# Performance work log

Measured on AMD Instinct MI355X. Metric: run time of the kernel, lower is better.

## Reference

```python
import jax, jax.numpy as jnp
import numpy as np

N, K, M = 1024, 256, 1024
INIT_SCALE = 0.1


def setup_inputs() -> dict:
    key = jax.random.key(0)
    kx, kw = jax.random.split(key)
    x = jax.random.normal(kx, (N, K), dtype=jnp.float32)
    weight = jax.random.normal(kw, (M, K), dtype=jnp.float32) * INIT_SCALE
    return {"x": x, "weight": weight}


def reference(x, weight):
    # Tropical (max-plus) matmul: out[n, m] = max_k(|x[n, k]| + |w[m, k]|)
    ax = jnp.abs(x)        # [N, K]
    aw = jnp.abs(weight)   # [M, K]
    # broadcast to [N, M, K] then reduce over K (mirrors the original expand+add+max)
    return jnp.max(ax[:, None, :] + aw[None, :, :], axis=2)  # [N, M]
```

## Files before the change

### kernel.cpp

```cpp
#include <hip/hip_runtime.h>


typedef float v2f __attribute__((ext_vector_type(2)));
typedef float v4f __attribute__((ext_vector_type(4)));

constexpr int TILE  = 32;
constexpr int KB    = 64;
constexpr int KKP   = KB / 2;
constexpr int PITCH = TILE + 2;

__global__ void __launch_bounds__(256)
tropical_kernel(const float* __restrict__ xg, const float* __restrict__ wg,
                float* __restrict__ outg)
{
    constexpr int K = 256;
    constexpr int M = 1024;

    __shared__ __align__(16) v2f xs[KKP * PITCH];
    __shared__ __align__(16) v2f ws[KKP * PITCH];

    const int tid = threadIdx.x;
    const int tx = tid & 15;
    const int ty = tid >> 4;
    const int bn = (int)(blockIdx.x >> 5) * TILE;
    const int bm = (int)(blockIdx.x & 31) * TILE;

    const int r = tid >> 3;
    const int c = (tid & 7) * 8;
    const float* xbase = xg + (bn + r) * K + c;
    const float* wbase = wg + (bm + r) * K + c;

    v4f xr0 = *(const v4f*)(xbase);
    v4f xr1 = *(const v4f*)(xbase + 4);
    v4f wr0 = *(const v4f*)(wbase);
    v4f wr1 = *(const v4f*)(wbase + 4);

    float a00 = 0.f, a01 = 0.f, a10 = 0.f, a11 = 0.f;

    const int kp = c >> 1;

    for (int chunk = 0; chunk < K / KB; ++chunk) {
        __syncthreads();
        xs[(kp + 0) * PITCH + r] = (v2f){fabsf(xr0.x), fabsf(xr0.y)};
        xs[(kp + 1) * PITCH + r] = (v2f){fabsf(xr0.z), fabsf(xr0.w)};
        xs[(kp + 2) * PITCH + r] = (v2f){fabsf(xr1.x), fabsf(xr1.y)};
        xs[(kp + 3) * PITCH + r] = (v2f){fabsf(xr1.z), fabsf(xr1.w)};
        ws[(kp + 0) * PITCH + r] = (v2f){fabsf(wr0.x), fabsf(wr0.y)};
        ws[(kp + 1) * PITCH + r] = (v2f){fabsf(wr0.z), fabsf(wr0.w)};
        ws[(kp + 2) * PITCH + r] = (v2f){fabsf(wr1.x), fabsf(wr1.y)};
        ws[(kp + 3) * PITCH + r] = (v2f){fabsf(wr1.z), fabsf(wr1.w)};
        __syncthreads();

        if (chunk + 1 < K / KB) {
            const float* xn = xbase + (chunk + 1) * KB;
            const float* wn = wbase + (chunk + 1) * KB;
            xr0 = *(const v4f*)(xn);
            xr1 = *(const v4f*)(xn + 4);
            wr0 = *(const v4f*)(wn);
            wr1 = *(const v4f*)(wn + 4);
        }

#pragma unroll
        for (int kk = 0; kk < KKP; ++kk) {
            v4f xv = *(const v4f*)&xs[kk * PITCH + 2 * ty];
            v4f wv = *(const v4f*)&ws[kk * PITCH + 2 * tx];
            v2f x0 = {xv.x, xv.y}, x1 = {xv.z, xv.w};
            v2f w0 = {wv.x, wv.y}, w1 = {wv.z, wv.w};
            v2f s;
            s = x0 + w0; a00 = fmaxf(a00, fmaxf(s.x, s.y));
            s = x0 + w1; a01 = fmaxf(a01, fmaxf(s.x, s.y));
            s = x1 + w0; a10 = fmaxf(a10, fmaxf(s.x, s.y));
            s = x1 + w1; a11 = fmaxf(a11, fmaxf(s.x, s.y));
        }
    }

    const int n0 = bn + 2 * ty;
    const int m0 = bm + 2 * tx;
    *(v2f*)(outg + n0 * M + m0)       = (v2f){a00, a01};
    *(v2f*)(outg + (n0 + 1) * M + m0) = (v2f){a10, a11};
}

extern "C" void kernel_launch(void* const* d_in, const int* in_sizes, int n_in,
                              void* d_out, int out_size, void* d_ws, size_t ws_size,
                              hipStream_t stream)
{
    const float* x = (const float*)d_in[0];
    const float* w = (const float*)d_in[1];
    float* out = (float*)d_out;

    dim3 grid(1024);
    dim3 block(256);
    tropical_kernel<<<grid, block, 0, stream>>>(x, w, out);
}
```

Baseline: 71.13 us.

## Use 64x64 tiles with 4x4 per-thread outputs and full-K XOR-swizzled LDS

Block tile grows from 32x32 to 64x64, and each thread now computes a 4x4 output micro-tile instead of 2x2. The whole K=256 slice of x and w is staged into LDS once, with an XOR swizzle in place of padding, so the chunked K loop and its repeated barriers go away. This raises arithmetic intensity per LDS read and cuts synchronization. In exchange, LDS per block reaches 128KB, the grid drops to 256 blocks, and occupancy is limited to one block per CU.

Result: slower. 72.57 us (+2.0%).

```diff
diff --git a/kernel.cpp b/kernel.cpp
--- a/kernel.cpp
+++ b/kernel.cpp
@@ -4,80 +4,100 @@
 typedef float v2f __attribute__((ext_vector_type(2)));
 typedef float v4f __attribute__((ext_vector_type(4)));
 
-constexpr int TILE  = 32;
-constexpr int KB    = 64;
-constexpr int KKP   = KB / 2;
-constexpr int PITCH = TILE + 2;
+constexpr int K    = 256;
+constexpr int M    = 1024;
+constexpr int TILE = 64;
+constexpr int KP   = K / 2;
+constexpr int P    = TILE;
 
-__global__ void __launch_bounds__(256)
+__global__ void __launch_bounds__(256, 1)
 tropical_kernel(const float* __restrict__ xg, const float* __restrict__ wg,
                 float* __restrict__ outg)
 {
-    constexpr int K = 256;
-    constexpr int M = 1024;
-
-    __shared__ __align__(16) v2f xs[KKP * PITCH];
-    __shared__ __align__(16) v2f ws[KKP * PITCH];
+    __shared__ __align__(16) v2f xs[KP * P];
+    __shared__ __align__(16) v2f ws[KP * P];
 
     const int tid = threadIdx.x;
-    const int tx = tid & 15;
-    const int ty = tid >> 4;
-    const int bn = (int)(blockIdx.x >> 5) * TILE;
-    const int bm = (int)(blockIdx.x & 31) * TILE;
+    const int tx  = tid & 15;
+    const int ty  = tid >> 4;
+    const int bn  = (int)(blockIdx.x >> 4) * TILE;
+    const int bm  = (int)(blockIdx.x & 15) * TILE;
 
-    const int r = tid >> 3;
-    const int c = (tid & 7) * 8;
-    const float* xbase = xg + (bn + r) * K + c;
-    const float* wbase = wg + (bm + r) * K + c;
+    const int r0 = tid >> 3;
+    const int l  = tid & 7;
 
-    v4f xr0 = *(const v4f*)(xbase);
-    v4f xr1 = *(const v4f*)(xbase + 4);
-    v4f wr0 = *(const v4f*)(wbase);
-    v4f wr1 = *(const v4f*)(wbase + 4);
-
-    float a00 = 0.f, a01 = 0.f, a10 = 0.f, a11 = 0.f;
-
-    const int kp = c >> 1;
-
-    for (int chunk = 0; chunk < K / KB; ++chunk) {
-        __syncthreads();
-        xs[(kp + 0) * PITCH + r] = (v2f){fabsf(xr0.x), fabsf(xr0.y)};
-        xs[(kp + 1) * PITCH + r] = (v2f){fabsf(xr0.z), fabsf(xr0.w)};
-        xs[(kp + 2) * PITCH + r] = (v2f){fabsf(xr1.x), fabsf(xr1.y)};
-        xs[(kp + 3) * PITCH + r] = (v2f){fabsf(xr1.z), fabsf(xr1.w)};
-        ws[(kp + 0) * PITCH + r] = (v2f){fabsf(wr0.x), fabsf(wr0.y)};
-        ws[(kp + 1) * PITCH + r] = (v2f){fabsf(wr0.z), fabsf(wr0.w)};
-        ws[(kp + 2) * PITCH + r] = (v2f){fabsf(wr1.x), fabsf(wr1.y)};
-        ws[(kp + 3) * PITCH + r] = (v2f){fabsf(wr1.z), fabsf(wr1.w)};
-        __syncthreads();
-
-        if (chunk + 1 < K / KB) {
-            const float* xn = xbase + (chunk + 1) * KB;
-            const float* wn = wbase + (chunk + 1) * KB;
-            xr0 = *(const v4f*)(xn);
-            xr1 = *(const v4f*)(xn + 4);
-            wr0 = *(const v4f*)(wn);
-            wr1 = *(const v4f*)(wn + 4);
-        }
+    const float* xr0 = xg + (bn + r0) * K;
+    const float* xr1 = xg + (bn + r0 + 32) * K;
+    const float* wr0 = wg + (bm + r0) * K;
+    const float* wr1 = wg + (bm + r0 + 32) * K;
 
 #pragma unroll
-        for (int kk = 0; kk < KKP; ++kk) {
-            v4f xv = *(const v4f*)&xs[kk * PITCH + 2 * ty];
-            v4f wv = *(const v4f*)&ws[kk * PITCH + 2 * tx];
-            v2f x0 = {xv.x, xv.y}, x1 = {xv.z, xv.w};
-            v2f w0 = {wv.x, wv.y}, w1 = {wv.z, wv.w};
-            v2f s;
-            s = x0 + w0; a00 = fmaxf(a00, fmaxf(s.x, s.y));
-            s = x0 + w1; a01 = fmaxf(a01, fmaxf(s.x, s.y));
-            s = x1 + w0; a10 = fmaxf(a10, fmaxf(s.x, s.y));
-            s = x1 + w1; a11 = fmaxf(a11, fmaxf(s.x, s.y));
-        }
+    for (int i = 0; i < 8; ++i) {
+        const int q  = l + 8 * i;
+        const int kp = 2 * q;
+        v4f a = *(const v4f*)(xr0 + 4 * q);
+        v4f b = *(const v4f*)(xr1 + 4 * q);
+        v4f c = *(const v4f*)(wr0 + 4 * q);
+        v4f d = *(const v4f*)(wr1 + 4 * q);
+        const int s0 = ((kp    ) & 3) << 2;
+        const int s1 = ((kp + 1) & 3) << 2;
+        xs[(kp    ) * P + ((r0     ) ^ s0)] = (v2f){fabsf(a.x), fabsf(a.y)};
+        xs[(kp + 1) * P + ((r0     ) ^ s1)] = (v2f){fabsf(a.z), fabsf(a.w)};
+        xs[(kp    ) * P + ((r0 + 32) ^ s0)] = (v2f){fabsf(b.x), fabsf(b.y)};
+        xs[(kp + 1) * P + ((r0 + 32) ^ s1)] = (v2f){fabsf(b.z), fabsf(b.w)};
+        ws[(kp    ) * P + ((r0     ) ^ s0)] = (v2f){fabsf(c.x), fabsf(c.y)};
+        ws[(kp + 1) * P + ((r0     ) ^ s1)] = (v2f){fabsf(c.z), fabsf(c.w)};
+        ws[(kp    ) * P + ((r0 + 32) ^ s0)] = (v2f){fabsf(d.x), fabsf(d.y)};
+        ws[(kp + 1) * P + ((r0 + 32) ^ s1)] = (v2f){fabsf(d.z), fabsf(d.w)};
     }
 
-    const int n0 = bn + 2 * ty;
-    const int m0 = bm + 2 * tx;
-    *(v2f*)(outg + n0 * M + m0)       = (v2f){a00, a01};
-    *(v2f*)(outg + (n0 + 1) * M + m0) = (v2f){a10, a11};
+    __syncthreads();
+
+    float acc[4][4];
+#pragma unroll
+    for (int a2 = 0; a2 < 4; ++a2)
+#pragma unroll
+        for (int b2 = 0; b2 < 4; ++b2) acc[a2][b2] = 0.f;
+
+    int xo[4], wo[4];
+#pragma unroll
+    for (int c4 = 0; c4 < 4; ++c4) {
+        xo[c4] = (4 * ty) ^ (c4 << 2);
+        wo[c4] = (4 * tx) ^ (c4 << 2);
+    }
+
+#pragma unroll 4
+    for (int kp = 0; kp < KP; ++kp) {
+        const v2f* xrow = &xs[kp * P];
+        const v2f* wrow = &ws[kp * P];
+        const int xof = xo[kp & 3];
+        const int wof = wo[kp & 3];
+        v4f x01 = *(const v4f*)(xrow + xof);
+        v4f x23 = *(const v4f*)(xrow + xof + 2);
+        v4f w01 = *(const v4f*)(wrow + wof);
+        v4f w23 = *(const v4f*)(wrow + wof + 2);
+
+        v2f xa[4] = {{x01.x, x01.y}, {x01.z, x01.w},
+                     {x23.x, x23.y}, {x23.z, x23.w}};
+        v2f wa[4] = {{w01.x, w01.y}, {w01.z, w01.w},
+                     {w23.x, w23.y}, {w23.z, w23.w}};
+
+#pragma unroll
+        for (int a2 = 0; a2 < 4; ++a2)
+#pragma unroll
+            for (int b2 = 0; b2 < 4; ++b2) {
+                v2f s = xa[a2] + wa[b2];
+                acc[a2][b2] = fmaxf(acc[a2][b2], fmaxf(s.x, s.y));
+            }
+    }
+
+    const int n0 = bn + 4 * ty;
+    const int m0 = bm + 4 * tx;
+#pragma unroll
+    for (int j = 0; j < 4; ++j) {
+        v4f o = {acc[j][0], acc[j][1], acc[j][2], acc[j][3]};
+        *(v4f*)(outg + (n0 + j) * M + m0) = o;
+    }
 }
 
 extern "C" void kernel_launch(void* const* d_in, const int* in_sizes, int n_in,
@@ -88,7 +108,7 @@
     const float* w = (const float*)d_in[1];
     float* out = (float*)d_out;
 
-    dim3 grid(1024);
+    dim3 grid(256);
     dim3 block(256);
     tropical_kernel<<<grid, block, 0, stream>>>(x, w, out);
 }
```
